# Kernel optimization log

Measured on AMD Instinct MI355X. Metric: run time of the kernel, lower is better.

The kernel has to match this reference:

```python
import jax, jax.numpy as jnp
import numpy as np

HIDDEN = 1024
N_HEADS = 16
HEAD_DIM = HIDDEN // N_HEADS  # 64
B, N = 2, 2048
SCALE = HIDDEN ** (-0.5)  # NOTE: original scales by full hidden_size, not head_dim


def setup_inputs() -> dict:
    key = jax.random.key(0)
    k1, k2 = jax.random.split(key)
    hidden_states = jax.random.normal(k1, (B, N, HIDDEN), dtype=jnp.float32)
    attention_mask = jnp.ones((B, N), dtype=jnp.int32)
    # per-head no-bias Linear(hidden -> 3*head_dim), stacked: [h, hidden, 3*head_dim]
    W_qkv = jax.random.normal(k2, (N_HEADS, HIDDEN, 3 * HEAD_DIM), dtype=jnp.float32) * (HIDDEN ** -0.5)
    return {"hidden_states": hidden_states, "attention_mask": attention_mask, "W_qkv": W_qkv}


def reference(hidden_states, attention_mask, W_qkv):
    # qkv: [b, h, n, 3*d]
    qkv = jnp.einsum('bnD,hDe->bhne', hidden_states, W_qkv)
    q, k, v = jnp.split(qkv, 3, axis=-1)  # each [b, h, n, d]
    scores = jnp.einsum('bhid,bhjd->bhij', q, k) * SCALE
    mask = attention_mask[:, None, None, :] == 0  # [b,1,1,n]
    scores = jnp.where(mask, -jnp.inf, scores)
    attn = jax.nn.softmax(scores, axis=-1)
    out = jnp.einsum('bhij,bhjd->bhid', attn, v)  # [b, h, n, d]
    # rearrange 'b h n d -> b n (h d)'
    return jnp.transpose(out, (0, 2, 1, 3)).reshape(out.shape[0], out.shape[2], -1)
```

## Files before the change

kernel.cpp:

```cpp
#include <hip/hip_runtime.h>
#include <hip/hip_bf16.h>


#define NH   16
#define HD   64
#define SEQ  2048
#define HID  1024
#define E3   192
#define QSCALE 0.04508422017f
#define MBIAS  -43.2808512f

typedef __attribute__((ext_vector_type(8))) short short8;
typedef __attribute__((ext_vector_type(4))) float f32x4;
typedef unsigned short ushort_t;

#define MFMA16(a, b, c) __builtin_amdgcn_mfma_f32_16x16x32_bf16((a), (b), (c), 0, 0, 0)

#if __has_builtin(__builtin_amdgcn_exp2f)
#define EXP2(x) __builtin_amdgcn_exp2f(x)
#else
#define EXP2(x) exp2f(x)
#endif

static __device__ __forceinline__ ushort_t f2bf(float x) {
    unsigned u = __builtin_bit_cast(unsigned, x);
    unsigned r = u + 0x7fff + ((u >> 16) & 1);
    return (ushort_t)(r >> 16);
}

static __device__ __forceinline__ unsigned pack_trunc(float hi, float lo) {
#if __has_builtin(__builtin_amdgcn_perm)
    return __builtin_amdgcn_perm(__builtin_bit_cast(unsigned, hi),
                                 __builtin_bit_cast(unsigned, lo), 0x07060302u);
#else
    return (__builtin_bit_cast(unsigned, hi) & 0xffff0000u) |
           (__builtin_bit_cast(unsigned, lo) >> 16);
#endif
}

static __device__ __forceinline__ void load_lds16(const void* g, void* l) {
    __builtin_amdgcn_global_load_lds(
        (__attribute__((address_space(1))) void*)(g),
        (__attribute__((address_space(3))) void*)(l), 16, 0, 0);
}

__global__ __launch_bounds__(256) void k_cvt_x(const void* __restrict__ Xv,
                                               ushort_t* __restrict__ Xb,
                                               int* __restrict__ flagp) {
    __shared__ int cnt;
    if (threadIdx.x == 0) cnt = 0;
    __syncthreads();
    const unsigned* X32 = (const unsigned*)Xv;
    if (threadIdx.x < 64) {
        unsigned u = X32[(size_t)blockIdx.x * 2048 + threadIdx.x * 32 + 7];
        int bexp = (u >> 7) & 0xFF;
        if (bexp >= 0x68 && bexp <= 0x90) atomicAdd(&cnt, 1);
    }
    __syncthreads();
    const int isf32 = (cnt < 32);
    if (blockIdx.x == 0 && threadIdx.x == 0) *flagp = isf32;

    const size_t base = ((size_t)blockIdx.x * 256 + threadIdx.x) * 16;
    if (isf32) {
        const float* Xf = (const float*)Xv;
        ushort_t tmp[16];
#pragma unroll
        for (int c = 0; c < 4; ++c) {
            float4 v = *(const float4*)(Xf + base + c * 4);
            tmp[c * 4 + 0] = f2bf(v.x); tmp[c * 4 + 1] = f2bf(v.y);
            tmp[c * 4 + 2] = f2bf(v.z); tmp[c * 4 + 3] = f2bf(v.w);
        }
        *(float4*)(Xb + base)     = ((const float4*)tmp)[0];
        *(float4*)(Xb + base + 8) = ((const float4*)tmp)[1];
    } else {
        const ushort_t* Xh = (const ushort_t*)Xv;
        *(float4*)(Xb + base)     = *(const float4*)(Xh + base);
        *(float4*)(Xb + base + 8) = *(const float4*)(Xh + base + 8);
    }
}

__global__ __launch_bounds__(256) void k_cvt_w(const void* __restrict__ Wv,
                                               ushort_t* __restrict__ Wt,
                                               const int* __restrict__ flagp) {
    __shared__ ushort_t tile[64][72];
    const int isf32 = *flagp;
    const int h  = blockIdx.x;
    const int dt = blockIdx.y;
    const int et = blockIdx.z;
    const int D0 = dt * 64, e0 = et * 64;
    const int t  = threadIdx.x;
#pragma unroll
    for (int r = 0; r < 2; ++r) {
        int row = r * 32 + (t >> 3);
        int col = (t & 7) * 8;
        size_t base = ((size_t)(h * HID + D0 + row)) * E3 + e0 + col;
        if (isf32) {
            const float* Wf = (const float*)Wv;
            float4 a = *(const float4*)(Wf + base);
            float4 c = *(const float4*)(Wf + base + 4);
            tile[row][col + 0] = f2bf(a.x); tile[row][col + 1] = f2bf(a.y);
            tile[row][col + 2] = f2bf(a.z); tile[row][col + 3] = f2bf(a.w);
            tile[row][col + 4] = f2bf(c.x); tile[row][col + 5] = f2bf(c.y);
            tile[row][col + 6] = f2bf(c.z); tile[row][col + 7] = f2bf(c.w);
        } else {
            *(float4*)&tile[row][col] = *(const float4*)((const ushort_t*)Wv + base);
        }
    }
    __syncthreads();
#pragma unroll
    for (int r = 0; r < 2; ++r) {
        int erow = r * 32 + (t >> 3);
        int dcol = (t & 7) * 8;
        ushort_t vals[8];
#pragma unroll
        for (int i = 0; i < 8; ++i) vals[i] = tile[dcol + i][erow];
        *(float4*)(Wt + ((size_t)(h * E3 + e0 + erow)) * HID + D0 + dcol) = *(float4*)vals;
    }
}

__global__ __launch_bounds__(256) void k_qkv(const ushort_t* __restrict__ Xb,
                                             const ushort_t* __restrict__ Wt,
                                             ushort_t* __restrict__ Qb,
                                             ushort_t* __restrict__ Kb,
                                             ushort_t* __restrict__ Vtb) {
    __shared__ __align__(16) ushort_t smem[2 * 128 * 64];
    ushort_t* Xl = smem;
    ushort_t* Wl = smem + 128 * 64;

    const int e0 = blockIdx.x * 128;
    const int m0 = blockIdx.y * 128;
    const int b  = m0 >> 11;
    const int n0 = m0 & 2047;
    const int t = threadIdx.x;
    const int w = t >> 6, lane = t & 63, l15 = lane & 15, quad = lane >> 4;
    const int wrow0 = (w & 1) * 64, wcol0 = (w >> 1) * 64;
    const int srow = lane >> 3;
    const int scb  = (lane & 7) ^ srow;

    f32x4 acc[4][4];
#pragma unroll
    for (int i = 0; i < 4; ++i)
#pragma unroll
        for (int j = 0; j < 4; ++j) acc[i][j] = (f32x4){0.f, 0.f, 0.f, 0.f};

    for (int k0 = 0; k0 < HID; k0 += 64) {
        __syncthreads();
#pragma unroll
        for (int cc = 0; cc < 4; ++cc) {
            const int ch  = w * 4 + cc;
            const int row = ch * 8 + srow;
            load_lds16(Xb + (size_t)(m0 + row) * HID + k0 + scb * 8, &Xl[ch * 512]);
            load_lds16(Wt + (size_t)(e0 + row) * HID + k0 + scb * 8, &Wl[ch * 512]);
        }
        __syncthreads();
#pragma unroll
        for (int kh = 0; kh < 2; ++kh) {
            short8 af[4], bfm[4];
#pragma unroll
            for (int i = 0; i < 4; ++i) {
                const int r = wrow0 + i * 16 + l15;
                af[i] = *(const short8*)&Xl[r * 64 + ((kh * 4 + quad) ^ (r & 7)) * 8];
            }
#pragma unroll
            for (int j = 0; j < 4; ++j) {
                const int r = wcol0 + j * 16 + l15;
                bfm[j] = *(const short8*)&Wl[r * 64 + ((kh * 4 + quad) ^ (r & 7)) * 8];
            }
#pragma unroll
            for (int i = 0; i < 4; ++i)
#pragma unroll
                for (int j = 0; j < 4; ++j)
                    acc[i][j] = MFMA16(af[i], bfm[j], acc[i][j]);
        }
    }

    ushort_t* Vbuf = smem;
    __syncthreads();
#pragma unroll
    for (int i = 0; i < 4; ++i) {
#pragma unroll
        for (int j = 0; j < 4; ++j) {
            const int E0v = e0 + wcol0 + j * 16;
            const int hh  = E0v / 192;
            const int r0  = E0v - hh * 192;
            const int bh  = b * NH + hh;
            const int nb  = n0 + wrow0 + i * 16 + quad * 4;
            if (r0 < 64) {
                const int e = r0 + l15;
#pragma unroll
                for (int reg = 0; reg < 4; ++reg)
                    Qb[((size_t)bh * SEQ + nb + reg) * HD + e] = f2bf(acc[i][j][reg] * QSCALE);
            } else if (r0 < 128) {
                const int e = r0 - 64 + l15;
#pragma unroll
                for (int reg = 0; reg < 4; ++reg)
                    Kb[((size_t)bh * SEQ + nb + reg) * HD + e] = f2bf(acc[i][j][reg]);
            } else {
                const int d  = r0 - 128 + l15;
                const int nl = wrow0 + i * 16 + quad * 4;
#pragma unroll
                for (int reg = 0; reg < 4; ++reg)
                    Vbuf[d * 136 + nl + reg] = f2bf(acc[i][j][reg]);
            }
        }
    }
    const int m3 = blockIdx.x % 3;
    if (m3 != 0) {
        __syncthreads();
        const int hv  = (e0 + ((m3 == 1) ? 0 : 64)) / 192;
        const int bhv = b * NH + hv;
        const int dr = t >> 2, part = t & 3;
        size_t dst = ((size_t)bhv * HD + dr) * SEQ + n0 + part * 32;
#pragma unroll
        for (int c = 0; c < 4; ++c) {
            float4 v = *(const float4*)&Vbuf[dr * 136 + part * 32 + c * 8];
            *(float4*)(Vtb + dst + c * 8) = v;
        }
    }
}

__global__ __launch_bounds__(512) void k_attn(const ushort_t* __restrict__ Qb,
                                              const ushort_t* __restrict__ Kb,
                                              const ushort_t* __restrict__ Vtb,
                                              const int* __restrict__ mask,
                                              void* __restrict__ outv,
                                              const int* __restrict__ flagp) {
    __shared__ __align__(16) char smem_raw[75776];
    ushort_t* Pl    = (ushort_t*)(smem_raw + 49152);
    float*    biasl = (float*)(smem_raw + 67584);

    const int isf32 = *flagp;
    const int q0 = blockIdx.x * 128;
    const int bh = blockIdx.y;
    const int b  = bh >> 4, h = bh & 15;
    const int t  = threadIdx.x;
    const int w  = t >> 6, lane = t & 63, l15 = lane & 15, quad = lane >> 4;
    const int srow = lane >> 3;
    const int scb  = (lane & 7) ^ srow;
    const int row8 = w * 8 + srow;

    const f32x4 zero4 = {0.f, 0.f, 0.f, 0.f};

#pragma unroll
    for (int tj = 0; tj < 2; ++tj) {
        ushort_t* kb = (ushort_t*)(smem_raw + tj * 16384);
        ushort_t* vb = kb + 4096;
        load_lds16(Kb  + ((size_t)bh * SEQ + tj * 64 + row8) * HD + scb * 8, &kb[w * 512]);
        load_lds16(Vtb + ((size_t)bh * HD + row8) * SEQ + tj * 64 + scb * 8, &vb[w * 512]);
    }

    int lm = 0;
    for (int i = t; i < SEQ; i += 512) {
        int mv = mask[b * SEQ + i];
        biasl[i] = mv ? 0.0f : MBIAS;
        lm |= (mv == 0);
    }
    const int qrow = q0 + w * 16 + l15;
    short8 qa0 = *(const short8*)(Qb + ((size_t)bh * SEQ + qrow) * HD + quad * 8);
    short8 qa1 = *(const short8*)(Qb + ((size_t)bh * SEQ + qrow) * HD + 32 + quad * 8);

    const int use_bias = __syncthreads_or(lm);

    f32x4 o[4];
#pragma unroll
    for (int mt = 0; mt < 4; ++mt) o[mt] = zero4;
    float l_r = 0.f;

    for (int j0 = 0; j0 < SEQ; j0 += 64) {
        const int idx = (j0 >> 6) % 3;
        if (j0 + 64 < SEQ) { asm volatile("s_waitcnt vmcnt(2)" ::: "memory"); }
        else               { asm volatile("s_waitcnt vmcnt(0)" ::: "memory"); }
        __builtin_amdgcn_s_barrier();
        asm volatile("" ::: "memory");
        if (j0 + 128 < SEQ) {
            ushort_t* kb = (ushort_t*)(smem_raw + ((idx + 2) % 3) * 16384);
            ushort_t* vb = kb + 4096;
            load_lds16(Kb  + ((size_t)bh * SEQ + j0 + 128 + row8) * HD + scb * 8, &kb[w * 512]);
            load_lds16(Vtb + ((size_t)bh * HD + row8) * SEQ + j0 + 128 + scb * 8, &vb[w * 512]);
        }
        ushort_t* kb = (ushort_t*)(smem_raw + idx * 16384);
        ushort_t* vb = kb + 4096;

        f32x4 s[4];
#pragma unroll
        for (int jt = 0; jt < 4; ++jt) {
            const int rk = jt * 16 + l15;
            short8 kb0 = *(const short8*)&kb[rk * 64 + ((quad)     ^ (rk & 7)) * 8];
            short8 kb1 = *(const short8*)&kb[rk * 64 + ((4 + quad) ^ (rk & 7)) * 8];
            s[jt] = MFMA16(kb0, qa0, zero4);
            s[jt] = MFMA16(kb1, qa1, s[jt]);
        }
        if (use_bias) {
#pragma unroll
            for (int jt = 0; jt < 4; ++jt) {
                float4 bj = *(const float4*)&biasl[j0 + jt * 16 + quad * 4];
#pragma unroll
                for (int reg = 0; reg < 4; ++reg)
                    s[jt][reg] += ((const float*)&bj)[reg];
            }
        }

#pragma unroll
        for (int jt = 0; jt < 4; ++jt) {
            float p0 = EXP2(s[jt][0]);
            float p1 = EXP2(s[jt][1]);
            float p2 = EXP2(s[jt][2]);
            float p3 = EXP2(s[jt][3]);
            l_r += (p0 + p1) + (p2 + p3);
            uint2 u;
            u.x = pack_trunc(p1, p0);
            u.y = pack_trunc(p3, p2);
            *(uint2*)&Pl[(w * 16 + l15) * 72 + jt * 16 + quad * 4] = u;
        }
        short8 pb0 = *(const short8*)&Pl[(w * 16 + l15) * 72 + quad * 8];
        short8 pb1 = *(const short8*)&Pl[(w * 16 + l15) * 72 + 32 + quad * 8];
#pragma unroll
        for (int mt = 0; mt < 4; ++mt) {
            const int rv = mt * 16 + l15;
            short8 va0 = *(const short8*)&vb[rv * 64 + ((quad)     ^ (rv & 7)) * 8];
            short8 va1 = *(const short8*)&vb[rv * 64 + ((4 + quad) ^ (rv & 7)) * 8];
            o[mt] = MFMA16(va0, pb0, o[mt]);
            o[mt] = MFMA16(va1, pb1, o[mt]);
        }
    }

    l_r += __shfl_xor(l_r, 16);
    l_r += __shfl_xor(l_r, 32);
    const float rinv = 1.0f / l_r;

    __syncthreads();
    const int r = t >> 2, part = t & 3;
    if (!isf32) {
        ushort_t* Ol = (ushort_t*)smem_raw;
#pragma unroll
        for (int mt = 0; mt < 4; ++mt) {
            uint2 u;
            u.x = (unsigned)f2bf(o[mt][0] * rinv) | ((unsigned)f2bf(o[mt][1] * rinv) << 16);
            u.y = (unsigned)f2bf(o[mt][2] * rinv) | ((unsigned)f2bf(o[mt][3] * rinv) << 16);
            *(uint2*)&Ol[(w * 16 + l15) * 72 + mt * 16 + quad * 4] = u;
        }
        __syncthreads();
        float4 v0 = *(const float4*)&Ol[r * 72 + part * 16];
        float4 v1 = *(const float4*)&Ol[r * 72 + part * 16 + 8];
        ushort_t* outp = (ushort_t*)outv;
        size_t dst = ((size_t)b * SEQ + q0 + r) * HID + h * HD + part * 16;
        *(float4*)(outp + dst)     = v0;
        *(float4*)(outp + dst + 8) = v1;
    } else {
        float* Olf = (float*)smem_raw;
#pragma unroll
        for (int mt = 0; mt < 4; ++mt)
#pragma unroll
            for (int reg = 0; reg < 4; ++reg)
                Olf[(w * 16 + l15) * 68 + mt * 16 + quad * 4 + reg] = o[mt][reg] * rinv;
        __syncthreads();
        float* outp = (float*)outv;
        size_t dst = ((size_t)b * SEQ + q0 + r) * HID + h * HD + part * 16;
#pragma unroll
        for (int c = 0; c < 4; ++c) {
            float4 v = *(const float4*)&Olf[r * 68 + part * 16 + c * 4];
            *(float4*)(outp + dst + c * 4) = v;
        }
    }
}

extern "C" void kernel_launch(void* const* d_in, const int* in_sizes, int n_in,
                              void* d_out, int out_size, void* d_ws, size_t ws_size,
                              hipStream_t stream) {
    const void* X    = d_in[0];
    const int*  mask = (const int*)d_in[1];
    const void* W    = d_in[2];

    char* ws = (char*)d_ws;
    ushort_t* Qb    = (ushort_t*)(ws);
    ushort_t* Kb    = (ushort_t*)(ws + 8388608);
    ushort_t* Vtb   = (ushort_t*)(ws + 16777216);
    ushort_t* Wtb   = (ushort_t*)(ws + 25165824);
    int*      flagp = (int*)(ws + 31457280);
    ushort_t* Xb    = (ushort_t*)d_out;

    k_cvt_x<<<1024, 256, 0, stream>>>(X, Xb, flagp);
    k_cvt_w<<<dim3(16, 16, 3), 256, 0, stream>>>(W, Wtb, flagp);
    k_qkv<<<dim3(24, 32), 256, 0, stream>>>(Xb, Wtb, Qb, Kb, Vtb);
    k_attn<<<dim3(16, 32), 512, 0, stream>>>(Qb, Kb, Vtb, mask, d_out, flagp);
}
```

Measured before the change: 176.9 us.

## Switch attention to 32x32x16 MFMA with 4 waves of 32 query rows

Rewrites the attention kernel to use 32x32x16 bf16 MFMA tiles, with each of 4 waves owning 32 query rows instead of 8 waves owning 16 rows. Block size drops from 512 to 256 threads, and each thread issues two K/V LDS loads per tile, with the vmcnt wait adjusted to match. The larger MFMA tile raises operand reuse and reduces LDS reads and instruction count per FLOP. In exchange it uses more accumulator registers and runs fewer waves per block, which can cut latency hiding.

```diff
diff --git a/kernel.cpp b/kernel.cpp
--- a/kernel.cpp
+++ b/kernel.cpp
@@ -10,11 +10,13 @@
 #define QSCALE 0.04508422017f
 #define MBIAS  -43.2808512f
 
-typedef __attribute__((ext_vector_type(8))) short short8;
-typedef __attribute__((ext_vector_type(4))) float f32x4;
+typedef __attribute__((ext_vector_type(8)))  short short8;
+typedef __attribute__((ext_vector_type(4)))  float f32x4;
+typedef __attribute__((ext_vector_type(16))) float f32x16;
 typedef unsigned short ushort_t;
 
 #define MFMA16(a, b, c) __builtin_amdgcn_mfma_f32_16x16x32_bf16((a), (b), (c), 0, 0, 0)
+#define MFMA32(a, b, c) __builtin_amdgcn_mfma_f32_32x32x16_bf16((a), (b), (c), 0, 0, 0)
 
 #if __has_builtin(__builtin_amdgcn_exp2f)
 #define EXP2(x) __builtin_amdgcn_exp2f(x)
@@ -219,7 +221,7 @@
     }
 }
 
-__global__ __launch_bounds__(512) void k_attn(const ushort_t* __restrict__ Qb,
+__global__ __launch_bounds__(256) void k_attn(const ushort_t* __restrict__ Qb,
                                               const ushort_t* __restrict__ Kb,
                                               const ushort_t* __restrict__ Vtb,
                                               const int* __restrict__ mask,
@@ -234,131 +236,160 @@
     const int bh = blockIdx.y;
     const int b  = bh >> 4, h = bh & 15;
     const int t  = threadIdx.x;
-    const int w  = t >> 6, lane = t & 63, l15 = lane & 15, quad = lane >> 4;
+    const int w  = t >> 6, lane = t & 63;
+    const int l31 = lane & 31, half = lane >> 5;
     const int srow = lane >> 3;
     const int scb  = (lane & 7) ^ srow;
-    const int row8 = w * 8 + srow;
-
-    const f32x4 zero4 = {0.f, 0.f, 0.f, 0.f};
+    const int prow = w * 32 + l31;
+
+    const f32x16 zero16 = {0.f,0.f,0.f,0.f,0.f,0.f,0.f,0.f,
+                           0.f,0.f,0.f,0.f,0.f,0.f,0.f,0.f};
 
 #pragma unroll
     for (int tj = 0; tj < 2; ++tj) {
         ushort_t* kb = (ushort_t*)(smem_raw + tj * 16384);
         ushort_t* vb = kb + 4096;
-        load_lds16(Kb  + ((size_t)bh * SEQ + tj * 64 + row8) * HD + scb * 8, &kb[w * 512]);
-        load_lds16(Vtb + ((size_t)bh * HD + row8) * SEQ + tj * 64 + scb * 8, &vb[w * 512]);
+#pragma unroll
+        for (int c = 0; c < 2; ++c) {
+            const int ch  = w * 2 + c;
+            const int row = ch * 8 + srow;
+            load_lds16(Kb  + ((size_t)bh * SEQ + tj * 64 + row) * HD + scb * 8, &kb[ch * 512]);
+            load_lds16(Vtb + ((size_t)bh * HD + row) * SEQ + tj * 64 + scb * 8, &vb[ch * 512]);
+        }
     }
 
     int lm = 0;
-    for (int i = t; i < SEQ; i += 512) {
+    for (int i = t; i < SEQ; i += 256) {
         int mv = mask[b * SEQ + i];
         biasl[i] = mv ? 0.0f : MBIAS;
         lm |= (mv == 0);
     }
-    const int qrow = q0 + w * 16 + l15;
-    short8 qa0 = *(const short8*)(Qb + ((size_t)bh * SEQ + qrow) * HD + quad * 8);
-    short8 qa1 = *(const short8*)(Qb + ((size_t)bh * SEQ + qrow) * HD + 32 + quad * 8);
+    short8 qa[4];
+#pragma unroll
+    for (int s = 0; s < 4; ++s)
+        qa[s] = *(const short8*)(Qb + ((size_t)bh * SEQ + q0 + prow) * HD + s * 16 + half * 8);
 
     const int use_bias = __syncthreads_or(lm);
 
-    f32x4 o[4];
-#pragma unroll
-    for (int mt = 0; mt < 4; ++mt) o[mt] = zero4;
+    f32x16 o[2];
+    o[0] = zero16; o[1] = zero16;
     float l_r = 0.f;
 
     for (int j0 = 0; j0 < SEQ; j0 += 64) {
         const int idx = (j0 >> 6) % 3;
-        if (j0 + 64 < SEQ) { asm volatile("s_waitcnt vmcnt(2)" ::: "memory"); }
+        if (j0 + 64 < SEQ) { asm volatile("s_waitcnt vmcnt(4)" ::: "memory"); }
         else               { asm volatile("s_waitcnt vmcnt(0)" ::: "memory"); }
         __builtin_amdgcn_s_barrier();
         asm volatile("" ::: "memory");
         if (j0 + 128 < SEQ) {
             ushort_t* kb = (ushort_t*)(smem_raw + ((idx + 2) % 3) * 16384);
             ushort_t* vb = kb + 4096;
-            load_lds16(Kb  + ((size_t)bh * SEQ + j0 + 128 + row8) * HD + scb * 8, &kb[w * 512]);
-            load_lds16(Vtb + ((size_t)bh * HD + row8) * SEQ + j0 + 128 + scb * 8, &vb[w * 512]);
+#pragma unroll
+            for (int c = 0; c < 2; ++c) {
+                const int ch  = w * 2 + c;
+                const int row = ch * 8 + srow;
+                load_lds16(Kb  + ((size_t)bh * SEQ + j0 + 128 + row) * HD + scb * 8, &kb[ch * 512]);
+                load_lds16(Vtb + ((size_t)bh * HD + row) * SEQ + j0 + 128 + scb * 8, &vb[ch * 512]);
+            }
         }
         ushort_t* kb = (ushort_t*)(smem_raw + idx * 16384);
         ushort_t* vb = kb + 4096;
 
-        f32x4 s[4];
-#pragma unroll
-        for (int jt = 0; jt < 4; ++jt) {
-            const int rk = jt * 16 + l15;
-            short8 kb0 = *(const short8*)&kb[rk * 64 + ((quad)     ^ (rk & 7)) * 8];
-            short8 kb1 = *(const short8*)&kb[rk * 64 + ((4 + quad) ^ (rk & 7)) * 8];
-            s[jt] = MFMA16(kb0, qa0, zero4);
-            s[jt] = MFMA16(kb1, qa1, s[jt]);
+        f32x16 st[2];
+#pragma unroll
+        for (int kt = 0; kt < 2; ++kt) {
+            const int rk = kt * 32 + l31;
+            st[kt] = zero16;
+#pragma unroll
+            for (int s = 0; s < 4; ++s) {
+                short8 ka = *(const short8*)&kb[rk * 64 + ((2 * s + half) ^ (rk & 7)) * 8];
+                st[kt] = MFMA32(ka, qa[s], st[kt]);
+            }
         }
         if (use_bias) {
 #pragma unroll
-            for (int jt = 0; jt < 4; ++jt) {
-                float4 bj = *(const float4*)&biasl[j0 + jt * 16 + quad * 4];
-#pragma unroll
-                for (int reg = 0; reg < 4; ++reg)
-                    s[jt][reg] += ((const float*)&bj)[reg];
-            }
-        }
-
-#pragma unroll
-        for (int jt = 0; jt < 4; ++jt) {
-            float p0 = EXP2(s[jt][0]);
-            float p1 = EXP2(s[jt][1]);
-            float p2 = EXP2(s[jt][2]);
-            float p3 = EXP2(s[jt][3]);
-            l_r += (p0 + p1) + (p2 + p3);
-            uint2 u;
-            u.x = pack_trunc(p1, p0);
-            u.y = pack_trunc(p3, p2);
-            *(uint2*)&Pl[(w * 16 + l15) * 72 + jt * 16 + quad * 4] = u;
-        }
-        short8 pb0 = *(const short8*)&Pl[(w * 16 + l15) * 72 + quad * 8];
-        short8 pb1 = *(const short8*)&Pl[(w * 16 + l15) * 72 + 32 + quad * 8];
-#pragma unroll
-        for (int mt = 0; mt < 4; ++mt) {
-            const int rv = mt * 16 + l15;
-            short8 va0 = *(const short8*)&vb[rv * 64 + ((quad)     ^ (rv & 7)) * 8];
-            short8 va1 = *(const short8*)&vb[rv * 64 + ((4 + quad) ^ (rv & 7)) * 8];
-            o[mt] = MFMA16(va0, pb0, o[mt]);
-            o[mt] = MFMA16(va1, pb1, o[mt]);
-        }
-    }
-
-    l_r += __shfl_xor(l_r, 16);
+            for (int kt = 0; kt < 2; ++kt)
+#pragma unroll
+                for (int g = 0; g < 4; ++g) {
+                    float4 bj = *(const float4*)&biasl[j0 + kt * 32 + g * 8 + 4 * half];
+#pragma unroll
+                    for (int i = 0; i < 4; ++i)
+                        st[kt][g * 4 + i] += ((const float*)&bj)[i];
+                }
+        }
+
+#pragma unroll
+        for (int kt = 0; kt < 2; ++kt) {
+            float p[16];
+#pragma unroll
+            for (int r = 0; r < 16; ++r) { p[r] = EXP2(st[kt][r]); l_r += p[r]; }
+#pragma unroll
+            for (int g = 0; g < 4; ++g) {
+                uint2 u;
+                u.x = pack_trunc(p[4 * g + 1], p[4 * g + 0]);
+                u.y = pack_trunc(p[4 * g + 3], p[4 * g + 2]);
+                *(uint2*)&Pl[prow * 72 + kt * 32 + g * 8 + 4 * half] = u;
+            }
+        }
+        short8 pb[4];
+#pragma unroll
+        for (int s = 0; s < 4; ++s)
+            pb[s] = *(const short8*)&Pl[prow * 72 + s * 16 + half * 8];
+
+#pragma unroll
+        for (int dt = 0; dt < 2; ++dt) {
+            const int rv = dt * 32 + l31;
+#pragma unroll
+            for (int s = 0; s < 4; ++s) {
+                short8 va = *(const short8*)&vb[rv * 64 + ((2 * s + half) ^ (rv & 7)) * 8];
+                o[dt] = MFMA32(va, pb[s], o[dt]);
+            }
+        }
+    }
+
     l_r += __shfl_xor(l_r, 32);
     const float rinv = 1.0f / l_r;
 
     __syncthreads();
-    const int r = t >> 2, part = t & 3;
+    const int r = t >> 1, part = t & 1;
     if (!isf32) {
         ushort_t* Ol = (ushort_t*)smem_raw;
 #pragma unroll
-        for (int mt = 0; mt < 4; ++mt) {
-            uint2 u;
-            u.x = (unsigned)f2bf(o[mt][0] * rinv) | ((unsigned)f2bf(o[mt][1] * rinv) << 16);
-            u.y = (unsigned)f2bf(o[mt][2] * rinv) | ((unsigned)f2bf(o[mt][3] * rinv) << 16);
-            *(uint2*)&Ol[(w * 16 + l15) * 72 + mt * 16 + quad * 4] = u;
-        }
+        for (int dt = 0; dt < 2; ++dt)
+#pragma unroll
+            for (int g = 0; g < 4; ++g) {
+                uint2 u;
+                u.x = (unsigned)f2bf(o[dt][4 * g + 0] * rinv) |
+                      ((unsigned)f2bf(o[dt][4 * g + 1] * rinv) << 16);
+                u.y = (unsigned)f2bf(o[dt][4 * g + 2] * rinv) |
+                      ((unsigned)f2bf(o[dt][4 * g + 3] * rinv) << 16);
+                *(uint2*)&Ol[prow * 72 + dt * 32 + g * 8 + 4 * half] = u;
+            }
         __syncthreads();
-        float4 v0 = *(const float4*)&Ol[r * 72 + part * 16];
-        float4 v1 = *(const float4*)&Ol[r * 72 + part * 16 + 8];
         ushort_t* outp = (ushort_t*)outv;
-        size_t dst = ((size_t)b * SEQ + q0 + r) * HID + h * HD + part * 16;
-        *(float4*)(outp + dst)     = v0;
-        *(float4*)(outp + dst + 8) = v1;
+        size_t dst = ((size_t)b * SEQ + q0 + r) * HID + h * HD + part * 32;
+#pragma unroll
+        for (int c = 0; c < 4; ++c) {
+            float4 v = *(const float4*)&Ol[r * 72 + part * 32 + c * 8];
+            *(float4*)(outp + dst + c * 8) = v;
+        }
     } else {
         float* Olf = (float*)smem_raw;
 #pragma unroll
-        for (int mt = 0; mt < 4; ++mt)
-#pragma unroll
-            for (int reg = 0; reg < 4; ++reg)
-                Olf[(w * 16 + l15) * 68 + mt * 16 + quad * 4 + reg] = o[mt][reg] * rinv;
+        for (int dt = 0; dt < 2; ++dt)
+#pragma unroll
+            for (int g = 0; g < 4; ++g) {
+                float2 v0 = {o[dt][4 * g + 0] * rinv, o[dt][4 * g + 1] * rinv};
+                float2 v1 = {o[dt][4 * g + 2] * rinv, o[dt][4 * g + 3] * rinv};
+                *(float2*)&Olf[prow * 68 + dt * 32 + g * 8 + 4 * half]     = v0;
+                *(float2*)&Olf[prow * 68 + dt * 32 + g * 8 + 4 * half + 2] = v1;
+            }
         __syncthreads();
         float* outp = (float*)outv;
-        size_t dst = ((size_t)b * SEQ + q0 + r) * HID + h * HD + part * 16;
-#pragma unroll
-        for (int c = 0; c < 4; ++c) {
-            float4 v = *(const float4*)&Olf[r * 68 + part * 16 + c * 4];
+        size_t dst = ((size_t)b * SEQ + q0 + r) * HID + h * HD + part * 32;
+#pragma unroll
+        for (int c = 0; c < 8; ++c) {
+            float4 v = *(const float4*)&Olf[r * 68 + part * 32 + c * 4];
             *(float4*)(outp + dst + c * 4) = v;
         }
     }
@@ -382,5 +413,5 @@
     k_cvt_x<<<1024, 256, 0, stream>>>(X, Xb, flagp);
     k_cvt_w<<<dim3(16, 16, 3), 256, 0, stream>>>(W, Wtb, flagp);
     k_qkv<<<dim3(24, 32), 256, 0, stream>>>(Xb, Wtb, Qb, Kb, Vtb);
-    k_attn<<<dim3(16, 32), 512, 0, stream>>>(Qb, Kb, Vtb, mask, d_out, flagp);
-}
+    k_attn<<<dim3(16, 32), 256, 0, stream>>>(Qb, Kb, Vtb, mask, d_out, flagp);
+}
```

Result: slower. 184.3 us (+4.2%).
